# Optimization experiments

Hardware: AMD Instinct MI355X
Metric: run time of the kernel (lower is better)

Reference implementation:

```python
import jax, jax.numpy as jnp
import numpy as np

FP8_E4M3_MAX = 448.0
BLOCK_SIZE = 128


def _block_quant_dequant_e4m3(x, block_size=BLOCK_SIZE):
    """Per-block (along last dim) FP8 E4M3 fake quantize: returns dequantized fp32."""
    M, K = x.shape
    nb = K // block_size
    xb = x.reshape(M, nb, block_size)
    amax = jnp.clip(jnp.max(jnp.abs(xb), axis=-1, keepdims=True), 1e-12, None)
    scale = FP8_E4M3_MAX / amax  # per-block scale, [M, nb, 1]
    q = jnp.clip(xb * scale, -FP8_E4M3_MAX, FP8_E4M3_MAX).astype(jnp.float8_e4m3fn)
    deq = q.astype(jnp.float32) / scale
    return deq.reshape(M, K)


def _dual_quantize_weight(w, block_size=BLOCK_SIZE):
    """TCFP-12 dual quantization: FP8 hi component + FP8-quantized residual (lo)."""
    w_hi = _block_quant_dequant_e4m3(w, block_size)
    residual = w - w_hi
    w_lo = _block_quant_dequant_e4m3(residual, block_size)
    return w_hi + w_lo


def setup_inputs() -> dict:
    key = jax.random.key(0)
    k1, k2, k3 = jax.random.split(key, 3)
    B, T, DIN, DOUT = 8, 4096, 1024, 1024
    x = jax.random.normal(k1, (B, T, DIN), dtype=jnp.float32)
    weight = jax.random.normal(k2, (DOUT, DIN), dtype=jnp.float32) * 0.02
    bias = jax.random.normal(k3, (DOUT,), dtype=jnp.float32) * 0.01
    return {"x": x, "weight": weight, "bias": bias}


def reference(x, weight, bias):
    # Block-quantize activations (fake-quant, per 128-col block, E4M3)
    B, T, DIN = x.shape
    x2d = x.reshape(-1, DIN)
    x_q = _block_quant_dequant_e4m3(x2d, BLOCK_SIZE)
    # Dual-quantize weight: hi + residual lo components
    w_q = _dual_quantize_weight(weight, BLOCK_SIZE)
    # Block-scaled GEMM (dequantized reference math) + bias
    out2d = x_q @ w_q.T + bias
    return out2d.reshape(B, T, -1)
```

## Files before the change

### kernel.cpp

```cpp
#include <hip/hip_runtime.h>
#include <hip/hip_bf16.h>

typedef __bf16 bf16x8 __attribute__((ext_vector_type(8)));
typedef float  f32x4  __attribute__((ext_vector_type(4)));

#define GLOAD_LDS16(gptr, lptr)                                                  \
  __builtin_amdgcn_global_load_lds(                                              \
      (const __attribute__((address_space(1))) void*)(gptr),                     \
      (__attribute__((address_space(3))) void*)(lptr), 16, 0, 0)

__device__ __forceinline__ unsigned short f2bf(float f) {
  __hip_bfloat16 h = __float2bfloat16(f);
  return __builtin_bit_cast(unsigned short, h);
}

__device__ __forceinline__ void fq4(float* __restrict__ v) {
  float am = fmaxf(fmaxf(fabsf(v[0]), fabsf(v[1])),
                   fmaxf(fabsf(v[2]), fabsf(v[3])));
  am = fmaxf(am, __shfl_xor(am, 1));
  am = fmaxf(am, __shfl_xor(am, 2));
  am = fmaxf(am, __shfl_xor(am, 4));
  am = fmaxf(am, __shfl_xor(am, 8));
  am = fmaxf(am, __shfl_xor(am, 16));
  am = fmaxf(am, 1e-12f);
  const float scale = 448.0f / am;
  const float inv   = am * (1.0f / 448.0f);
  float c0 = fminf(fmaxf(v[0] * scale, -448.0f), 448.0f);
  float c1 = fminf(fmaxf(v[1] * scale, -448.0f), 448.0f);
  float c2 = fminf(fmaxf(v[2] * scale, -448.0f), 448.0f);
  float c3 = fminf(fmaxf(v[3] * scale, -448.0f), 448.0f);
  int pk = __builtin_amdgcn_cvt_pk_fp8_f32(c0, c1, 0, false);
  pk = __builtin_amdgcn_cvt_pk_fp8_f32(c2, c3, pk, true);
  v[0] = __builtin_amdgcn_cvt_f32_fp8(pk, 0) * inv;
  v[1] = __builtin_amdgcn_cvt_f32_fp8(pk, 1) * inv;
  v[2] = __builtin_amdgcn_cvt_f32_fp8(pk, 2) * inv;
  v[3] = __builtin_amdgcn_cvt_f32_fp8(pk, 3) * inv;
}

__global__ __launch_bounds__(256) void quant_x_k(const float* __restrict__ x,
                                                 unsigned short* __restrict__ xq) {
  const size_t u = (size_t)blockIdx.x * 256 + threadIdx.x;
  float v[4];
  *(float4*)v = ((const float4*)x)[u];
  fq4(v);
  union { uint2 q; unsigned short s[4]; } pk;
#pragma unroll
  for (int e = 0; e < 4; ++e) pk.s[e] = f2bf(v[e]);
  ((uint2*)xq)[u] = pk.q;
}

__global__ __launch_bounds__(256) void quant_w_k(const float* __restrict__ w,
                                                 unsigned short* __restrict__ wq) {
  const size_t u = (size_t)blockIdx.x * 256 + threadIdx.x;
  float a[4], h[4], r[4];
  *(float4*)a = ((const float4*)w)[u];
#pragma unroll
  for (int i = 0; i < 4; ++i) h[i] = a[i];
  fq4(h);
#pragma unroll
  for (int i = 0; i < 4; ++i) r[i] = a[i] - h[i];
  fq4(r);
  union { uint2 q; unsigned short s[4]; } pk;
#pragma unroll
  for (int e = 0; e < 4; ++e) pk.s[e] = f2bf(h[e] + r[e]);
  ((uint2*)wq)[u] = pk.q;
}

#define BM 256
#define BN 256
#define BK 64

#define VM4()  asm volatile("s_waitcnt vmcnt(4)" ::: "memory")
#define VM2()  asm volatile("s_waitcnt vmcnt(2)" ::: "memory")
#define VM0()  asm volatile("s_waitcnt vmcnt(0)" ::: "memory")
#define LG0()  do { asm volatile("s_waitcnt lgkmcnt(0)" ::: "memory");           \
                    __builtin_amdgcn_sched_barrier(0); } while (0)
#define BAR()  __builtin_amdgcn_s_barrier()

__global__ __launch_bounds__(512, 2) void gemm_bt_bias(
    const unsigned short* __restrict__ A,
    const unsigned short* __restrict__ B,
    const float* __restrict__ bias,
    float* __restrict__ C,
    int M, int N, int K) {
  __shared__ unsigned short lds[65536];
  unsigned short* ldsA = lds;
  unsigned short* ldsB = lds + 32768;

  const int tid  = threadIdx.x;
  const int wv   = tid >> 6;
  const int lane = tid & 63;
  const int nbn  = N / BN;
  const int nbm  = M / BM;

  int bm, bn;
  if ((nbm & 7) == 0) {
    const int xcd = blockIdx.x & 7;
    const int j   = blockIdx.x >> 3;
    bn = j % nbn;
    bm = xcd * (nbm >> 3) + j / nbn;
  } else {
    bn = blockIdx.x % nbn;
    bm = blockIdx.x / nbn;
  }

  const int wr = wv >> 2;
  const int wc = wv & 3;

  f32x4  acc[8][4] = {};
  bf16x8 a[4][2], b01[2][2], b23[2][2];

  const int    srcChunk = ((lane & 7) ^ ((lane >> 3) & 7)) * 8;
  const size_t laneSrc  = (size_t)(lane >> 3) * K + srcChunk;
  const unsigned short* gA = A + (size_t)bm * BM * K + laneSrc;
  const unsigned short* gB = B + (size_t)bn * BN * K + laneSrc;
  const int lr0 = wv * 16, lr1 = wv * 16 + 8;
  auto arow = [](int mq, int lr) { return mq * 64 + (lr < 64 ? lr : 64 + lr); };
  auto brow = [](int v,  int lr) { return v * 32 + (lr >> 5) * 64 + (lr & 31); };
  const int rA[2][2] = {{arow(0, lr0), arow(0, lr1)}, {arow(1, lr0), arow(1, lr1)}};
  const int rB[2][2] = {{brow(0, lr0), brow(0, lr1)}, {brow(1, lr0), brow(1, lr1)}};

  auto stageA = [&](int buf, int mq, int kt) {
#pragma unroll
    for (int t = 0; t < 2; ++t) {
      const int rb = rA[mq][t];
      GLOAD_LDS16(gA + (size_t)rb * K + kt * BK,
                  ldsA + buf * 16384 + rb * 64 + lane * 8);
    }
  };
  auto stageB = [&](int buf, int v, int kt) {
#pragma unroll
    for (int t = 0; t < 2; ++t) {
      const int rb = rB[v][t];
      GLOAD_LDS16(gB + (size_t)rb * K + kt * BK,
                  ldsB + buf * 16384 + rb * 64 + lane * 8);
    }
  };

  const int fRow = lane & 15;
  const int q4   = lane >> 4;
  const int s8   = fRow & 7;
  const int sw0  = ((q4)     ^ s8) * 8;
  const int sw1  = ((4 + q4) ^ s8) * 8;
  const int aRO  = (wr * 128 + fRow) * 64;
  const int bRO  = (wc * 64  + fRow) * 64;

  auto dsA = [&](int buf, int mq) {
    const unsigned short* p = ldsA + buf * 16384 + aRO + mq * 4096;
#pragma unroll
    for (int m = 0; m < 4; ++m) {
      a[m][0] = *(const bf16x8*)(p + m * 1024 + sw0);
      a[m][1] = *(const bf16x8*)(p + m * 1024 + sw1);
    }
  };
  auto dsB = [&](int buf, int njp, bf16x8 (&bb)[2][2]) {
    const unsigned short* p = ldsB + buf * 16384 + bRO + njp * 2048;
#pragma unroll
    for (int n = 0; n < 2; ++n) {
      bb[n][0] = *(const bf16x8*)(p + n * 1024 + sw0);
      bb[n][1] = *(const bf16x8*)(p + n * 1024 + sw1);
    }
  };

  auto mm = [&](int mq, int njp, bf16x8 (&bb)[2][2]) {
    __builtin_amdgcn_s_setprio(1);
#pragma unroll
    for (int m = 0; m < 4; ++m)
#pragma unroll
      for (int n = 0; n < 2; ++n)
#pragma unroll
        for (int k = 0; k < 2; ++k)
          acc[mq * 4 + m][njp * 2 + n] = __builtin_amdgcn_mfma_f32_16x16x32_bf16(
              a[m][k], bb[n][k], acc[mq * 4 + m][njp * 2 + n], 0, 0, 0);
    __builtin_amdgcn_s_setprio(0);
  };

  stageA(0, 0, 0); stageB(0, 0, 0); stageB(0, 1, 0); stageA(0, 1, 0);
  VM4(); BAR();

  const int niter = K / (2 * BK);
  for (int i = 0; i < niter - 1; ++i) {
    const int t1 = 2 * i + 1, t2 = 2 * i + 2;
    dsA(0, 0); dsB(0, 0, b01); stageA(1, 0, t1);
    BAR(); LG0(); mm(0, 0, b01); VM4(); BAR();
    dsB(0, 1, b23); stageB(1, 0, t1);
    BAR(); LG0(); mm(0, 1, b23); VM4(); BAR();
    dsA(0, 1); stageB(1, 1, t1);
    BAR(); LG0(); mm(1, 0, b01); BAR();
    stageA(1, 1, t1);
    BAR(); mm(1, 1, b23); VM4(); BAR();
    dsA(1, 0); dsB(1, 0, b01); stageA(0, 0, t2);
    BAR(); LG0(); mm(0, 0, b01); VM4(); BAR();
    dsB(1, 1, b23); stageB(0, 0, t2);
    BAR(); LG0(); mm(0, 1, b23); VM4(); BAR();
    dsA(1, 1); stageB(0, 1, t2);
    BAR(); LG0(); mm(1, 0, b01); BAR();
    stageA(0, 1, t2);
    BAR(); mm(1, 1, b23); VM4(); BAR();
  }
  {
    const int t1 = 2 * niter - 1;
    dsA(0, 0); dsB(0, 0, b01); stageA(1, 0, t1);
    BAR(); LG0(); mm(0, 0, b01); VM4(); BAR();
    dsB(0, 1, b23); stageB(1, 0, t1);
    BAR(); LG0(); mm(0, 1, b23); VM4(); BAR();
    dsA(0, 1); stageB(1, 1, t1);
    BAR(); LG0(); mm(1, 0, b01); BAR();
    stageA(1, 1, t1);
    BAR(); mm(1, 1, b23); VM4(); BAR();
    dsA(1, 0); dsB(1, 0, b01);
    BAR(); LG0(); mm(0, 0, b01); VM2(); BAR();
    dsB(1, 1, b23);
    BAR(); LG0(); mm(0, 1, b23); VM0(); BAR();
    dsA(1, 1);
    BAR(); LG0(); mm(1, 0, b01); BAR();
    mm(1, 1, b23);
  }

  const int    n0 = bn * BN + wc * 64 + fRow;
  const size_t m0 = (size_t)bm * BM + wr * 128 + (q4 << 2);
#pragma unroll
  for (int nj = 0; nj < 4; ++nj) {
    const int col = n0 + nj * 16;
    const float bv = bias[col];
#pragma unroll
    for (int mi = 0; mi < 8; ++mi) {
      const size_t base = (m0 + (size_t)mi * 16) * N + col;
#pragma unroll
      for (int r = 0; r < 4; ++r)
        C[base + (size_t)r * N] = acc[mi][nj][r] + bv;
    }
  }
}

extern "C" void kernel_launch(void* const* d_in, const int* in_sizes, int n_in,
                              void* d_out, int out_size, void* d_ws, size_t ws_size,
                              hipStream_t stream) {
  const float* x    = (const float*)d_in[0];
  const float* w    = (const float*)d_in[1];
  const float* bias = (const float*)d_in[2];

  const int DOUT = in_sizes[2];
  const int DIN  = in_sizes[1] / DOUT;
  const int M    = in_sizes[0] / DIN;

  unsigned short* xq = (unsigned short*)d_ws;
  unsigned short* wq = xq + (size_t)M * DIN;

  hipLaunchKernelGGL(quant_x_k, dim3((size_t)M * DIN / 4 / 256), dim3(256), 0,
                     stream, x, xq);
  hipLaunchKernelGGL(quant_w_k, dim3((size_t)DOUT * DIN / 4 / 256), dim3(256), 0,
                     stream, w, wq);

  const int grid = (M / BM) * (DOUT / BN);
  hipLaunchKernelGGL(gemm_bt_bias, dim3(grid), dim3(512), 0, stream,
                     xq, wq, bias, (float*)d_out, M, DOUT, DIN);
}
```

Baseline: 307.6 us.

## Load GEMM B operand directly to registers and merge quant kernels

The GEMM stops staging the weight (B) tile through LDS. Each wave now loads its B fragments straight from global memory into double-buffered registers (even/odd sets), while A keeps the LDS path. This halves LDS use and removes the B ds_reads, at the cost of more VGPRs and uncoalesced, redundant global reads of B across waves. The two quantization kernels are also merged into a single launch to save one kernel launch.

```diff
diff --git a/kernel.cpp b/kernel.cpp
--- a/kernel.cpp
+++ b/kernel.cpp
@@ -37,44 +37,45 @@
   v[3] = __builtin_amdgcn_cvt_f32_fp8(pk, 3) * inv;
 }
 
-__global__ __launch_bounds__(256) void quant_x_k(const float* __restrict__ x,
-                                                 unsigned short* __restrict__ xq) {
-  const size_t u = (size_t)blockIdx.x * 256 + threadIdx.x;
-  float v[4];
-  *(float4*)v = ((const float4*)x)[u];
-  fq4(v);
-  union { uint2 q; unsigned short s[4]; } pk;
-#pragma unroll
-  for (int e = 0; e < 4; ++e) pk.s[e] = f2bf(v[e]);
-  ((uint2*)xq)[u] = pk.q;
-}
-
-__global__ __launch_bounds__(256) void quant_w_k(const float* __restrict__ w,
-                                                 unsigned short* __restrict__ wq) {
-  const size_t u = (size_t)blockIdx.x * 256 + threadIdx.x;
-  float a[4], h[4], r[4];
-  *(float4*)a = ((const float4*)w)[u];
-#pragma unroll
-  for (int i = 0; i < 4; ++i) h[i] = a[i];
-  fq4(h);
-#pragma unroll
-  for (int i = 0; i < 4; ++i) r[i] = a[i] - h[i];
-  fq4(r);
-  union { uint2 q; unsigned short s[4]; } pk;
-#pragma unroll
-  for (int e = 0; e < 4; ++e) pk.s[e] = f2bf(h[e] + r[e]);
-  ((uint2*)wq)[u] = pk.q;
+__global__ __launch_bounds__(256) void quant_xw(const float* __restrict__ x,
+                                                unsigned short* __restrict__ xq,
+                                                const float* __restrict__ w,
+                                                unsigned short* __restrict__ wq,
+                                                int nwBlocks) {
+  if ((int)blockIdx.x < nwBlocks) {
+    const size_t u = (size_t)blockIdx.x * 256 + threadIdx.x;
+    float a[4], h[4], r[4];
+    *(float4*)a = ((const float4*)w)[u];
+#pragma unroll
+    for (int i = 0; i < 4; ++i) h[i] = a[i];
+    fq4(h);
+#pragma unroll
+    for (int i = 0; i < 4; ++i) r[i] = a[i] - h[i];
+    fq4(r);
+    union { uint2 q; unsigned short s[4]; } pk;
+#pragma unroll
+    for (int e = 0; e < 4; ++e) pk.s[e] = f2bf(h[e] + r[e]);
+    ((uint2*)wq)[u] = pk.q;
+  } else {
+    const size_t u = (size_t)(blockIdx.x - nwBlocks) * 256 + threadIdx.x;
+    float v[4];
+    *(float4*)v = ((const float4*)x)[u];
+    fq4(v);
+    union { uint2 q; unsigned short s[4]; } pk;
+#pragma unroll
+    for (int e = 0; e < 4; ++e) pk.s[e] = f2bf(v[e]);
+    ((uint2*)xq)[u] = pk.q;
+  }
 }
 
 #define BM 256
 #define BN 256
 #define BK 64
 
-#define VM4()  asm volatile("s_waitcnt vmcnt(4)" ::: "memory")
-#define VM2()  asm volatile("s_waitcnt vmcnt(2)" ::: "memory")
-#define VM0()  asm volatile("s_waitcnt vmcnt(0)" ::: "memory")
+#define VMG(n) asm volatile("s_waitcnt vmcnt(" #n ")" ::: "memory")
 #define LG0()  do { asm volatile("s_waitcnt lgkmcnt(0)" ::: "memory");           \
                     __builtin_amdgcn_sched_barrier(0); } while (0)
+#define SB0()  __builtin_amdgcn_sched_barrier(0)
 #define BAR()  __builtin_amdgcn_s_barrier()
 
 __global__ __launch_bounds__(512, 2) void gemm_bt_bias(
@@ -83,9 +84,7 @@
     const float* __restrict__ bias,
     float* __restrict__ C,
     int M, int N, int K) {
-  __shared__ unsigned short lds[65536];
-  unsigned short* ldsA = lds;
-  unsigned short* ldsB = lds + 32768;
+  __shared__ unsigned short ldsA[2 * BM * BK];
 
   const int tid  = threadIdx.x;
   const int wv   = tid >> 6;
@@ -108,17 +107,15 @@
   const int wc = wv & 3;
 
   f32x4  acc[8][4] = {};
-  bf16x8 a[4][2], b01[2][2], b23[2][2];
+  bf16x8 a[4][2];
+  bf16x8 b01e[2][2], b23e[2][2], b01o[2][2], b23o[2][2];
 
   const int    srcChunk = ((lane & 7) ^ ((lane >> 3) & 7)) * 8;
   const size_t laneSrc  = (size_t)(lane >> 3) * K + srcChunk;
   const unsigned short* gA = A + (size_t)bm * BM * K + laneSrc;
-  const unsigned short* gB = B + (size_t)bn * BN * K + laneSrc;
   const int lr0 = wv * 16, lr1 = wv * 16 + 8;
   auto arow = [](int mq, int lr) { return mq * 64 + (lr < 64 ? lr : 64 + lr); };
-  auto brow = [](int v,  int lr) { return v * 32 + (lr >> 5) * 64 + (lr & 31); };
   const int rA[2][2] = {{arow(0, lr0), arow(0, lr1)}, {arow(1, lr0), arow(1, lr1)}};
-  const int rB[2][2] = {{brow(0, lr0), brow(0, lr1)}, {brow(1, lr0), brow(1, lr1)}};
 
   auto stageA = [&](int buf, int mq, int kt) {
 #pragma unroll
@@ -126,14 +123,6 @@
       const int rb = rA[mq][t];
       GLOAD_LDS16(gA + (size_t)rb * K + kt * BK,
                   ldsA + buf * 16384 + rb * 64 + lane * 8);
-    }
-  };
-  auto stageB = [&](int buf, int v, int kt) {
-#pragma unroll
-    for (int t = 0; t < 2; ++t) {
-      const int rb = rB[v][t];
-      GLOAD_LDS16(gB + (size_t)rb * K + kt * BK,
-                  ldsB + buf * 16384 + rb * 64 + lane * 8);
     }
   };
 
@@ -143,7 +132,6 @@
   const int sw0  = ((q4)     ^ s8) * 8;
   const int sw1  = ((4 + q4) ^ s8) * 8;
   const int aRO  = (wr * 128 + fRow) * 64;
-  const int bRO  = (wc * 64  + fRow) * 64;
 
   auto dsA = [&](int buf, int mq) {
     const unsigned short* p = ldsA + buf * 16384 + aRO + mq * 4096;
@@ -153,68 +141,63 @@
       a[m][1] = *(const bf16x8*)(p + m * 1024 + sw1);
     }
   };
-  auto dsB = [&](int buf, int njp, bf16x8 (&bb)[2][2]) {
-    const unsigned short* p = ldsB + buf * 16384 + bRO + njp * 2048;
-#pragma unroll
-    for (int n = 0; n < 2; ++n) {
-      bb[n][0] = *(const bf16x8*)(p + n * 1024 + sw0);
-      bb[n][1] = *(const bf16x8*)(p + n * 1024 + sw1);
-    }
-  };
-
-  auto mm = [&](int mq, int njp, bf16x8 (&bb)[2][2]) {
+
+  const unsigned short* gBr =
+      B + (size_t)(bn * BN + wc * 64 + fRow) * K + q4 * 8;
+  auto loadB = [&](int kt, int njp, bf16x8 (&bb)[2][2]) {
+#pragma unroll
+    for (int n = 0; n < 2; ++n)
+#pragma unroll
+      for (int kk = 0; kk < 2; ++kk)
+        bb[n][kk] = *(const bf16x8*)(gBr + (size_t)((njp * 2 + n) * 16) * K +
+                                     kt * BK + kk * 32);
+  };
+
+  auto mm32 = [&](int mq, bf16x8 (&b01)[2][2], bf16x8 (&b23)[2][2]) {
     __builtin_amdgcn_s_setprio(1);
 #pragma unroll
     for (int m = 0; m < 4; ++m)
 #pragma unroll
-      for (int n = 0; n < 2; ++n)
-#pragma unroll
-        for (int k = 0; k < 2; ++k)
-          acc[mq * 4 + m][njp * 2 + n] = __builtin_amdgcn_mfma_f32_16x16x32_bf16(
-              a[m][k], bb[n][k], acc[mq * 4 + m][njp * 2 + n], 0, 0, 0);
+      for (int kk = 0; kk < 2; ++kk) {
+        acc[mq * 4 + m][0] = __builtin_amdgcn_mfma_f32_16x16x32_bf16(
+            a[m][kk], b01[0][kk], acc[mq * 4 + m][0], 0, 0, 0);
+        acc[mq * 4 + m][1] = __builtin_amdgcn_mfma_f32_16x16x32_bf16(
+            a[m][kk], b01[1][kk], acc[mq * 4 + m][1], 0, 0, 0);
+        acc[mq * 4 + m][2] = __builtin_amdgcn_mfma_f32_16x16x32_bf16(
+            a[m][kk], b23[0][kk], acc[mq * 4 + m][2], 0, 0, 0);
+        acc[mq * 4 + m][3] = __builtin_amdgcn_mfma_f32_16x16x32_bf16(
+            a[m][kk], b23[1][kk], acc[mq * 4 + m][3], 0, 0, 0);
+      }
     __builtin_amdgcn_s_setprio(0);
   };
 
-  stageA(0, 0, 0); stageB(0, 0, 0); stageB(0, 1, 0); stageA(0, 1, 0);
-  VM4(); BAR();
-
-  const int niter = K / (2 * BK);
-  for (int i = 0; i < niter - 1; ++i) {
-    const int t1 = 2 * i + 1, t2 = 2 * i + 2;
-    dsA(0, 0); dsB(0, 0, b01); stageA(1, 0, t1);
-    BAR(); LG0(); mm(0, 0, b01); VM4(); BAR();
-    dsB(0, 1, b23); stageB(1, 0, t1);
-    BAR(); LG0(); mm(0, 1, b23); VM4(); BAR();
-    dsA(0, 1); stageB(1, 1, t1);
-    BAR(); LG0(); mm(1, 0, b01); BAR();
-    stageA(1, 1, t1);
-    BAR(); mm(1, 1, b23); VM4(); BAR();
-    dsA(1, 0); dsB(1, 0, b01); stageA(0, 0, t2);
-    BAR(); LG0(); mm(0, 0, b01); VM4(); BAR();
-    dsB(1, 1, b23); stageB(0, 0, t2);
-    BAR(); LG0(); mm(0, 1, b23); VM4(); BAR();
-    dsA(1, 1); stageB(0, 1, t2);
-    BAR(); LG0(); mm(1, 0, b01); BAR();
-    stageA(0, 1, t2);
-    BAR(); mm(1, 1, b23); VM4(); BAR();
+  stageA(0, 0, 0); stageA(0, 1, 0); SB0();
+  loadB(0, 0, b01e); loadB(0, 1, b23e); SB0();
+  VMG(8);
+  BAR();
+
+  const int ntile = K / BK;
+  for (int i = 0; i < ntile / 2 - 1; ++i) {
+    const int to = 2 * i + 1, te = 2 * i + 2;
+    dsA(0, 0); stageA(1, 0, to); SB0(); loadB(to, 0, b01o); SB0();
+    BAR(); LG0(); mm32(0, b01e, b23e); VMG(10); BAR();
+    dsA(0, 1); stageA(1, 1, to); SB0(); loadB(to, 1, b23o); SB0();
+    BAR(); LG0(); mm32(1, b01e, b23e); VMG(10); BAR();
+    dsA(1, 0); stageA(0, 0, te); SB0(); loadB(te, 0, b01e); SB0();
+    BAR(); LG0(); mm32(0, b01o, b23o); VMG(10); BAR();
+    dsA(1, 1); stageA(0, 1, te); SB0(); loadB(te, 1, b23e); SB0();
+    BAR(); LG0(); mm32(1, b01o, b23o); VMG(10); BAR();
   }
   {
-    const int t1 = 2 * niter - 1;
-    dsA(0, 0); dsB(0, 0, b01); stageA(1, 0, t1);
-    BAR(); LG0(); mm(0, 0, b01); VM4(); BAR();
-    dsB(0, 1, b23); stageB(1, 0, t1);
-    BAR(); LG0(); mm(0, 1, b23); VM4(); BAR();
-    dsA(0, 1); stageB(1, 1, t1);
-    BAR(); LG0(); mm(1, 0, b01); BAR();
-    stageA(1, 1, t1);
-    BAR(); mm(1, 1, b23); VM4(); BAR();
-    dsA(1, 0); dsB(1, 0, b01);
-    BAR(); LG0(); mm(0, 0, b01); VM2(); BAR();
-    dsB(1, 1, b23);
-    BAR(); LG0(); mm(0, 1, b23); VM0(); BAR();
+    const int to = ntile - 1;
+    dsA(0, 0); stageA(1, 0, to); SB0(); loadB(to, 0, b01o); SB0();
+    BAR(); LG0(); mm32(0, b01e, b23e); VMG(10); BAR();
+    dsA(0, 1); stageA(1, 1, to); SB0(); loadB(to, 1, b23o); SB0();
+    BAR(); LG0(); mm32(1, b01e, b23e); VMG(10); BAR();
+    dsA(1, 0);
+    BAR(); LG0(); mm32(0, b01o, b23o); VMG(0); BAR();
     dsA(1, 1);
-    BAR(); LG0(); mm(1, 0, b01); BAR();
-    mm(1, 1, b23);
+    BAR(); LG0(); mm32(1, b01o, b23o);
   }
 
   const int    n0 = bn * BN + wc * 64 + fRow;
@@ -247,10 +230,10 @@
   unsigned short* xq = (unsigned short*)d_ws;
   unsigned short* wq = xq + (size_t)M * DIN;
 
-  hipLaunchKernelGGL(quant_x_k, dim3((size_t)M * DIN / 4 / 256), dim3(256), 0,
-                     stream, x, xq);
-  hipLaunchKernelGGL(quant_w_k, dim3((size_t)DOUT * DIN / 4 / 256), dim3(256), 0,
-                     stream, w, wq);
+  const int nw = (DOUT * DIN / 4) / 256;
+  const int nx = (int)((size_t)M * DIN / 4 / 256);
+  hipLaunchKernelGGL(quant_xw, dim3(nw + nx), dim3(256), 0, stream,
+                     x, xq, w, wq, nw);
 
   const int grid = (M / BM) * (DOUT / BN);
   hipLaunchKernelGGL(gemm_bt_bias, dim3(grid), dim3(512), 0, stream,
```

After: 357.0 us. 16.0% more time.
